# Performance work log

Measured on AMD Instinct MI355X. Metric: run time of the kernel, lower is better.

Reference implementation:

```python
import jax, jax.numpy as jnp
import numpy as np

DIM = 768
NUM_HEADS = 12
HEAD_DIM = DIM // NUM_HEADS
SCALE = HEAD_DIM ** -0.5
EPS = 1e-6


def setup_inputs() -> dict:
    key = jax.random.key(0)
    k_x, k_p, k_qkv, k_proj = jax.random.split(key, 4)
    B, N = 16, 577
    x = jax.random.normal(k_x, (B, N, DIM), dtype=jnp.float32)
    # binary keep/drop policy per token (as produced by an upstream gumbel gate)
    policy = jax.random.randint(k_p, (B, N, 1), 0, 2).astype(jnp.float32)
    Wqkv = jax.random.normal(k_qkv, (DIM, 3 * DIM), dtype=jnp.float32) * 0.02
    bqkv = jnp.zeros((3 * DIM,), dtype=jnp.float32)
    Wproj = jax.random.normal(k_proj, (DIM, DIM), dtype=jnp.float32) * 0.02
    bproj = jnp.zeros((DIM,), dtype=jnp.float32)
    return {"x": x, "policy": policy, "Wqkv": Wqkv, "bqkv": bqkv,
            "Wproj": Wproj, "bproj": bproj}


def reference(x, policy, Wqkv, bqkv, Wproj, bproj):
    B, N, C = x.shape
    # qkv projection -> [3, B, H, N, Dh]
    qkv = (x @ Wqkv + bqkv).reshape(B, N, 3, NUM_HEADS, HEAD_DIM)
    qkv = jnp.transpose(qkv, (2, 0, 3, 1, 4))
    q, k, v = qkv[0], qkv[1], qkv[2]
    # scaled attention logits [B, H, N, N]
    attn = jnp.einsum("bhnd,bhmd->bhnm", q, k) * SCALE
    # policy-masked softmax (training-mode formula: eye keeps self-attention alive)
    ap = policy.reshape(B, 1, 1, N)
    eye = jnp.eye(N, dtype=ap.dtype).reshape(1, 1, N, N)
    ap = ap + (1.0 - ap) * eye
    max_att = jnp.max(attn, axis=-1, keepdims=True)
    e = jnp.exp(attn - max_att) * ap
    attn = (e + EPS / N) / (jnp.sum(e, axis=-1, keepdims=True) + EPS)
    # attend and project
    out = jnp.einsum("bhnm,bhmd->bhnd", attn, v)
    out = jnp.transpose(out, (0, 2, 1, 3)).reshape(B, N, C)
    return out @ Wproj + bproj
```

## Files before the change

kernel.cpp:

```cpp
#include <hip/hip_runtime.h>
#include <hip/hip_bf16.h>

#define QKVC   2304
#define NHEAD  12
#define NTOK   577
#define NBATCH 16
#define NROWS  (NBATCH * NTOK)
#define NPAD   640
#define SCALE  0.125f
#define EPSV   1e-6f

typedef __bf16  bf16x8 __attribute__((ext_vector_type(8)));
typedef float   f32x4  __attribute__((ext_vector_type(4)));

__device__ __forceinline__ unsigned short f2bf(float f) {
    union { float f; unsigned u; } v; v.f = f;
    unsigned r = v.u + 0x7FFFu + ((v.u >> 16) & 1u);
    return (unsigned short)(r >> 16);
}
__device__ __forceinline__ unsigned short f2bf_trunc(float f) {
    return (unsigned short)(__float_as_uint(f) >> 16);
}
__device__ __forceinline__ f32x4 mfma16(bf16x8 a, bf16x8 b, f32x4 c) {
    return __builtin_amdgcn_mfma_f32_16x16x32_bf16(a, b, c, 0, 0, 0);
}

#define GLDS16(g, l) __builtin_amdgcn_global_load_lds( \
    (const __attribute__((address_space(1))) unsigned int*)(g), \
    (__attribute__((address_space(3))) unsigned int*)(l), 16, 0, 0)

__device__ void transpose_tile(const float* __restrict__ src, unsigned short* __restrict__ dst,
                               int K, int N, int bx, int by, int t) {
    __shared__ unsigned short lt[64 * 72];
    int n0 = bx * 64, k0 = by * 64;
    int kk = t >> 4, nn = (t & 15) * 4;
    for (int i = 0; i < 4; i++) {
        int kr = kk + i * 16;
        float4 v = *(const float4*)&src[(size_t)(k0 + kr) * N + n0 + nn];
        lt[(nn + 0) * 72 + kr] = f2bf(v.x);
        lt[(nn + 1) * 72 + kr] = f2bf(v.y);
        lt[(nn + 2) * 72 + kr] = f2bf(v.z);
        lt[(nn + 3) * 72 + kr] = f2bf(v.w);
    }
    __syncthreads();
    int n = t >> 2, seg = (t & 3) * 16;
    uint4 a = *(uint4*)&lt[n * 72 + seg];
    uint4 b = *(uint4*)&lt[n * 72 + seg + 8];
    *(uint4*)&dst[(size_t)(n0 + n) * K + k0 + seg]     = a;
    *(uint4*)&dst[(size_t)(n0 + n) * K + k0 + seg + 8] = b;
}

#define NCONV (NROWS * 768 / 4 / 256)
__global__ void k_prep(const float* __restrict__ x, unsigned short* __restrict__ xb,
                       const float* __restrict__ Wqkv, unsigned short* __restrict__ wqkvt,
                       const float* __restrict__ Wproj, unsigned short* __restrict__ wprojt) {
    int id = blockIdx.x, t = threadIdx.x;
    if (id < NCONV) {
        int idx = id * 256 + t;
        float4 v = ((const float4*)x)[idx];
        ushort4 o;
        o.x = f2bf(v.x); o.y = f2bf(v.y); o.z = f2bf(v.z); o.w = f2bf(v.w);
        ((ushort4*)xb)[idx] = o;
    } else if (id < NCONV + 432) {
        int i2 = id - NCONV;
        transpose_tile(Wqkv, wqkvt, 768, QKVC, i2 % 36, i2 / 36, t);
    } else {
        int i2 = id - NCONV - 432;
        transpose_tile(Wproj, wprojt, 768, 768, i2 % 12, i2 / 12, t);
    }
}

template <bool F32OUT>
__global__ __launch_bounds__(512, 2)
void k_gemm(const unsigned short* __restrict__ A, const unsigned short* __restrict__ B,
            const float* __restrict__ bias, void* __restrict__ outp, int Ncols,
            unsigned short* __restrict__ vt) {
    __shared__ unsigned short SL[49152];
    int t = threadIdx.x;
    int lane = t & 63, wave = t >> 6, quad = lane >> 4, l15 = lane & 15;
    int wm = wave >> 2, wn = wave & 3;
    int nT = Ncols >> 7;
    int nwg = gridDim.x;

    int q8 = nwg >> 3, r8 = nwg & 7;
    int xcd = blockIdx.x & 7, idx = blockIdx.x >> 3;
    int wg = (xcd < r8 ? xcd * (q8 + 1) : r8 * (q8 + 1) + (xcd - r8) * q8) + idx;
    int m0 = (wg / nT) * 256;
    int n0 = (wg % nT) * 128;

    int srow = lane >> 2;
    int sseg = (lane & 3) ^ ((lane >> 3) & 3);
    const unsigned short* gA0 = A + (size_t)(m0 +       wave * 16 + srow) * 768 + sseg * 8;
    const unsigned short* gA1 = A + (size_t)(m0 + 128 + wave * 16 + srow) * 768 + sseg * 8;
    const unsigned short* gB0 = B + (size_t)(n0 +       wave * 16 + srow) * 768 + sseg * 8;

    f32x4 acc[8][2] = {};

    auto STAGE = [&](int sx) {
        unsigned sa = (unsigned)(sx & 3) * 8192u + (unsigned)wave * 512u;
        unsigned sb = 32768u + (unsigned)(sx & 3) * 4096u + (unsigned)wave * 512u;
        int ko = sx * 32;
        GLDS16(gA0 + ko, &SL[sa]);
        GLDS16(gA1 + ko, &SL[sa + 4096]);
        GLDS16(gB0 + ko, &SL[sb]);
    };

    auto STEP = [&](int s, bool stage) {
        unsigned ab = (unsigned)(s & 3) * 8192u;
        unsigned bb = 32768u + (unsigned)(s & 3) * 4096u;
        unsigned ro = (unsigned)(quad ^ ((l15 >> 1) & 3)) * 8u;
        bf16x8 af[8], bfr[2];
        #pragma unroll
        for (int i = 0; i < 8; i++)
            af[i]  = *(const bf16x8*)&SL[ab + (unsigned)(wm * 128 + i * 16 + l15) * 32u + ro];
        #pragma unroll
        for (int i = 0; i < 2; i++)
            bfr[i] = *(const bf16x8*)&SL[bb + (unsigned)(wn * 32 + i * 16 + l15) * 32u + ro];
        if (stage) STAGE(s + 3);
        asm volatile("s_waitcnt lgkmcnt(0)" ::: "memory");
        __builtin_amdgcn_s_setprio(1);
        #pragma unroll
        for (int mi = 0; mi < 8; mi++)
            #pragma unroll
            for (int ni = 0; ni < 2; ni++)
                acc[mi][ni] = mfma16(af[mi], bfr[ni], acc[mi][ni]);
        __builtin_amdgcn_s_setprio(0);
    };

    STAGE(0); STAGE(1); STAGE(2);
    for (int s = 0; s < 21; s++) {
        asm volatile("s_waitcnt vmcnt(6)" ::: "memory");
        asm volatile("s_barrier" ::: "memory");
        STEP(s, true);
    }
    asm volatile("s_waitcnt vmcnt(6)" ::: "memory");
    asm volatile("s_barrier" ::: "memory");
    STEP(21, false);
    asm volatile("s_waitcnt vmcnt(3)" ::: "memory");
    asm volatile("s_barrier" ::: "memory");
    STEP(22, false);
    asm volatile("s_waitcnt vmcnt(0)" ::: "memory");
    asm volatile("s_barrier" ::: "memory");
    STEP(23, false);

    if constexpr (F32OUT) {
        for (int ni = 0; ni < 2; ni++) {
            int col = n0 + wn * 32 + ni * 16 + l15;
            float bv = bias[col];
            for (int mi = 0; mi < 8; mi++) {
                int rowm = m0 + wm * 128 + mi * 16 + quad * 4;
                for (int r = 0; r < 4; r++) {
                    int m = rowm + r;
                    if (m < NROWS)
                        ((float*)outp)[(size_t)m * Ncols + col] = acc[mi][ni][r] + bv;
                }
            }
        }
    } else {
        __syncthreads();
        for (int ni = 0; ni < 2; ni++) {
            int colL = wn * 32 + ni * 16 + l15;
            float bv = bias[n0 + colL];
            for (int mi = 0; mi < 8; mi++) {
                int rowL = wm * 128 + mi * 16 + quad * 4;
                for (int r = 0; r < 4; r++)
                    SL[(rowL + r) * 136 + colL] = f2bf(acc[mi][ni][r] + bv);
            }
        }
        __syncthreads();
        if (n0 < 1536) {
            for (int rr = 0; rr < 8; rr++) {
                int row = rr * 32 + (t >> 4);
                int m = m0 + row;
                if (m < NROWS) {
                    uint4 v = *(uint4*)&SL[row * 136 + (t & 15) * 8];
                    *(uint4*)&((unsigned short*)outp)[(size_t)m * Ncols + n0 + (t & 15) * 8] = v;
                }
            }
        } else {
            int h0 = (n0 - 1536) >> 6;
            for (int i = 0; i < 16; i++) {
                int c = wave * 16 + i;
                int h = h0 + (c >> 6), d = c & 63;
                for (int half = 0; half < 4; half++) {
                    int lr = half * 64 + lane;
                    int m = m0 + lr;
                    if (m < NROWS) {
                        unsigned bbx = (unsigned)m / 577u;
                        int tok = m - (int)bbx * 577;
                        vt[(((size_t)bbx * NHEAD + h) * 64 + d) * NPAD + tok] =
                            SL[lr * 136 + c];
                    }
                }
            }
        }
    }
}

__global__ __launch_bounds__(256, 4)
void k_attn(const unsigned short* __restrict__ qkv, const unsigned short* __restrict__ vt,
            const float* __restrict__ policy, unsigned short* __restrict__ ao) {
    __shared__ unsigned short Ks[64 * 72];
    __shared__ unsigned short Vs[64 * 72];
    __shared__ unsigned short Ps[4][32 * 72];
    __shared__ float pol[NPAD];
    int t = threadIdx.x;
    int lane = t & 63, wave = t >> 6, quad = lane >> 4, l15 = lane & 15;
    int b = blockIdx.z, h = blockIdx.y, qt = blockIdx.x;
    const unsigned short* qbase = qkv + (size_t)(b * NTOK) * QKVC + h * 64;
    const unsigned short* kbase = qkv + (size_t)(b * NTOK) * QKVC + 768 + h * 64;
    const unsigned short* vbase = vt + (size_t)(b * NHEAD + h) * 64 * NPAD;

    for (int i = t; i < NPAD; i += 256)
        pol[i] = (i < NTOK) ? policy[b * NTOK + i] : 0.f;

    bf16x8 qf[2][2];
    for (int mi = 0; mi < 2; mi++) {
        const unsigned short* qp =
            qbase + (size_t)(qt * 128 + mi * 64 + wave * 16 + l15) * QKVC + quad * 8;
        qf[mi][0] = *(const bf16x8*)qp;
        qf[mi][1] = *(const bf16x8*)(qp + 32);
    }
    bf16x8 onesf;
    for (int j = 0; j < 8; j++) onesf[j] = (__bf16)1.0f;
    f32x4 o[2][4] = {};
    f32x4 ls[2] = {};
    int rowtok0[2];
    for (int mi = 0; mi < 2; mi++)
        rowtok0[mi] = qt * 128 + mi * 64 + wave * 16 + quad * 4;
    __syncthreads();

    for (int kt = 0; kt < 10; kt++) {
        int key0 = kt * 64;
        for (int i = t; i < 512; i += 256) {
            int row = i >> 3, seg = (i & 7) * 8;
            *(uint4*)&Ks[row * 72 + seg] = *(const uint4*)&kbase[(size_t)(key0 + row) * QKVC + seg];
            *(uint4*)&Vs[row * 72 + seg] = *(const uint4*)&vbase[(size_t)row * NPAD + key0 + seg];
        }
        __syncthreads();

        for (int ci = 0; ci < 4; ci++) {
            bf16x8 kf0 = *(const bf16x8*)&Ks[(ci * 16 + l15) * 72 + quad * 8];
            bf16x8 kf1 = *(const bf16x8*)&Ks[(ci * 16 + l15) * 72 + 32 + quad * 8];
            int col = key0 + ci * 16 + l15;
            float pc = pol[col];
            for (int mi = 0; mi < 2; mi++) {
                f32x4 a = {};
                a = mfma16(qf[mi][0], kf0, a);
                a = mfma16(qf[mi][1], kf1, a);
                for (int r = 0; r < 4; r++) {
                    float ap = (col == rowtok0[mi] + r) ? 1.f : pc;
                    float e = __expf(a[r] * SCALE) * ap;
                    Ps[wave][(mi * 16 + quad * 4 + r) * 72 + ci * 16 + l15] = f2bf_trunc(e);
                }
            }
        }
        __asm__ volatile("s_waitcnt lgkmcnt(0)" ::: "memory");
        bf16x8 pf[2][2];
        for (int mi = 0; mi < 2; mi++) {
            pf[mi][0] = *(const bf16x8*)&Ps[wave][(mi * 16 + l15) * 72 + quad * 8];
            pf[mi][1] = *(const bf16x8*)&Ps[wave][(mi * 16 + l15) * 72 + 32 + quad * 8];
            ls[mi] = mfma16(pf[mi][0], onesf, ls[mi]);
            ls[mi] = mfma16(pf[mi][1], onesf, ls[mi]);
        }
        for (int di = 0; di < 4; di++) {
            bf16x8 vf0 = *(const bf16x8*)&Vs[(di * 16 + l15) * 72 + quad * 8];
            bf16x8 vf1 = *(const bf16x8*)&Vs[(di * 16 + l15) * 72 + 32 + quad * 8];
            for (int mi = 0; mi < 2; mi++) {
                o[mi][di] = mfma16(pf[mi][0], vf0, o[mi][di]);
                o[mi][di] = mfma16(pf[mi][1], vf1, o[mi][di]);
            }
        }
        __syncthreads();
    }

    for (int mi = 0; mi < 2; mi++) {
        for (int r = 0; r < 4; r++) {
            int tok = rowtok0[mi] + r;
            if (tok < NTOK) {
                float inv = __builtin_amdgcn_rcpf(ls[mi][r] + EPSV);
                for (int di = 0; di < 4; di++) {
                    float val = o[mi][di][r] * inv;
                    ao[((size_t)(b * NTOK + tok)) * 768 + h * 64 + di * 16 + l15] = f2bf(val);
                }
            }
        }
    }
}

extern "C" void kernel_launch(void* const* d_in, const int* in_sizes, int n_in,
                              void* d_out, int out_size, void* d_ws, size_t ws_size,
                              hipStream_t stream) {
    const float* x      = (const float*)d_in[0];
    const float* policy = (const float*)d_in[1];
    const float* Wqkv   = (const float*)d_in[2];
    const float* bqkv   = (const float*)d_in[3];
    const float* Wproj  = (const float*)d_in[4];
    const float* bproj  = (const float*)d_in[5];
    float* out = (float*)d_out;

    unsigned short* p = (unsigned short*)d_ws;
    unsigned short* xb     = p;
    unsigned short* ao     = p; p += (size_t)NROWS * 768;
    unsigned short* wqkvt  = p; p += (size_t)QKVC * 768;
    unsigned short* wprojt = p; p += (size_t)768 * 768;
    unsigned short* qkvb   = p; p += (size_t)NROWS * QKVC;
    unsigned short* vt     = p; p += (size_t)NBATCH * NHEAD * 64 * NPAD;

    int mT = (NROWS + 255) / 256;

    k_prep<<<NCONV + 432 + 144, 256, 0, stream>>>(x, xb, Wqkv, wqkvt, Wproj, wprojt);
    k_gemm<false><<<mT * (QKVC / 128), 512, 0, stream>>>(
        xb, wqkvt, bqkv, (void*)qkvb, QKVC, vt);
    k_attn<<<dim3(NPAD / 128, NHEAD, NBATCH), 256, 0, stream>>>(qkvb, vt, policy, ao);
    k_gemm<true><<<mT * (768 / 128), 512, 0, stream>>>(
        ao, wprojt, bproj, (void*)out, 768, nullptr);
}
```

Before: 206.7 us.

## Pre-tile GEMM operands into swizzled 16x32 chunks and use triple-buffered staging

The x conversion, weight transposes and the attention output now write GEMM operands in a pre-tiled, pre-swizzled layout of contiguous 16-row by 32-k chunks. Each wave's global-to-LDS load then reads one contiguous 1 KB block instead of strided row segments. The GEMM pipeline drops from four LDS stages to three, which cuts LDS use and may allow more occupancy, at the cost of less prefetch depth. The attention epilogue now does scattered scalar stores into the tiled layout.

```diff
diff --git a/kernel.cpp b/kernel.cpp
--- a/kernel.cpp
+++ b/kernel.cpp
@@ -9,6 +9,8 @@
 #define NPAD   640
 #define SCALE  0.125f
 #define EPSV   1e-6f
+#define KT     24
+#define CH     512
 
 typedef __bf16  bf16x8 __attribute__((ext_vector_type(8)));
 typedef float   f32x4  __attribute__((ext_vector_type(4)));
@@ -21,6 +23,9 @@
 __device__ __forceinline__ unsigned short f2bf_trunc(float f) {
     return (unsigned short)(__float_as_uint(f) >> 16);
 }
+__device__ __forceinline__ unsigned pack2bf(float a, float b) {
+    return (unsigned)f2bf(a) | ((unsigned)f2bf(b) << 16);
+}
 __device__ __forceinline__ f32x4 mfma16(bf16x8 a, bf16x8 b, f32x4 c) {
     return __builtin_amdgcn_mfma_f32_16x16x32_bf16(a, b, c, 0, 0, 0);
 }
@@ -29,8 +34,9 @@
     (const __attribute__((address_space(1))) unsigned int*)(g), \
     (__attribute__((address_space(3))) unsigned int*)(l), 16, 0, 0)
 
+
 __device__ void transpose_tile(const float* __restrict__ src, unsigned short* __restrict__ dst,
-                               int K, int N, int bx, int by, int t) {
+                               int N, int bx, int by, int t) {
     __shared__ unsigned short lt[64 * 72];
     int n0 = bx * 64, k0 = by * 64;
     int kk = t >> 4, nn = (t & 15) * 4;
@@ -43,30 +49,52 @@
         lt[(nn + 3) * 72 + kr] = f2bf(v.w);
     }
     __syncthreads();
-    int n = t >> 2, seg = (t & 3) * 16;
-    uint4 a = *(uint4*)&lt[n * 72 + seg];
-    uint4 b = *(uint4*)&lt[n * 72 + seg + 8];
-    *(uint4*)&dst[(size_t)(n0 + n) * K + k0 + seg]     = a;
-    *(uint4*)&dst[(size_t)(n0 + n) * K + k0 + seg + 8] = b;
-}
-
-#define NCONV (NROWS * 768 / 4 / 256)
-__global__ void k_prep(const float* __restrict__ x, unsigned short* __restrict__ xb,
+    int n = t >> 2;
+    int ks = (t & 3) * 16;
+    int gn = n0 + n;
+    int ntile = gn >> 4, r = gn & 15, s = (r >> 1) & 3;
+    for (int j = 0; j < 2; j++) {
+        int k = k0 + ks + j * 8;
+        int kt = k >> 5;
+        int q = ((k >> 3) & 3) ^ s;
+        uint4 v = *(uint4*)&lt[n * 72 + ks + j * 8];
+        *(uint4*)&dst[((size_t)ntile * KT + kt) * CH + r * 32 + q * 8] = v;
+    }
+}
+
+#define NCHUNK (577 * KT)
+#define CONVB  ((NCHUNK + 15) / 16)
+__global__ void k_prep(const float* __restrict__ x, unsigned short* __restrict__ xbt,
                        const float* __restrict__ Wqkv, unsigned short* __restrict__ wqkvt,
                        const float* __restrict__ Wproj, unsigned short* __restrict__ wprojt) {
     int id = blockIdx.x, t = threadIdx.x;
-    if (id < NCONV) {
-        int idx = id * 256 + t;
-        float4 v = ((const float4*)x)[idx];
-        ushort4 o;
-        o.x = f2bf(v.x); o.y = f2bf(v.y); o.z = f2bf(v.z); o.w = f2bf(v.w);
-        ((ushort4*)xb)[idx] = o;
-    } else if (id < NCONV + 432) {
-        int i2 = id - NCONV;
-        transpose_tile(Wqkv, wqkvt, 768, QKVC, i2 % 36, i2 / 36, t);
+    if (id < CONVB) {
+        int cid = id * 16 + (t >> 4);
+        if (cid < NCHUNK) {
+            int r = t & 15;
+            int mt = cid / KT, kt = cid - mt * KT;
+            const float* src = x + ((size_t)mt * 16 + r) * 768 + kt * 32;
+            int s = (r >> 1) & 3;
+            unsigned short* dst = xbt + (size_t)cid * CH + r * 32;
+            #pragma unroll
+            for (int q = 0; q < 4; q++) {
+                int g = q ^ s;
+                float4 v0 = *(const float4*)(src + g * 8);
+                float4 v1 = *(const float4*)(src + g * 8 + 4);
+                uint4 u;
+                u.x = pack2bf(v0.x, v0.y);
+                u.y = pack2bf(v0.z, v0.w);
+                u.z = pack2bf(v1.x, v1.y);
+                u.w = pack2bf(v1.z, v1.w);
+                *(uint4*)(dst + q * 8) = u;
+            }
+        }
+    } else if (id < CONVB + 432) {
+        int i2 = id - CONVB;
+        transpose_tile(Wqkv, wqkvt, QKVC, i2 % 36, i2 / 36, t);
     } else {
-        int i2 = id - NCONV - 432;
-        transpose_tile(Wproj, wprojt, 768, 768, i2 % 12, i2 / 12, t);
+        int i2 = id - CONVB - 432;
+        transpose_tile(Wproj, wprojt, 768, i2 % 12, i2 / 12, t);
     }
 }
 
@@ -75,7 +103,7 @@
 void k_gemm(const unsigned short* __restrict__ A, const unsigned short* __restrict__ B,
             const float* __restrict__ bias, void* __restrict__ outp, int Ncols,
             unsigned short* __restrict__ vt) {
-    __shared__ unsigned short SL[49152];
+    __shared__ unsigned short SL[36864];
     int t = threadIdx.x;
     int lane = t & 63, wave = t >> 6, quad = lane >> 4, l15 = lane & 15;
     int wm = wave >> 2, wn = wave & 3;
@@ -88,26 +116,23 @@
     int m0 = (wg / nT) * 256;
     int n0 = (wg % nT) * 128;
 
-    int srow = lane >> 2;
-    int sseg = (lane & 3) ^ ((lane >> 3) & 3);
-    const unsigned short* gA0 = A + (size_t)(m0 +       wave * 16 + srow) * 768 + sseg * 8;
-    const unsigned short* gA1 = A + (size_t)(m0 + 128 + wave * 16 + srow) * 768 + sseg * 8;
-    const unsigned short* gB0 = B + (size_t)(n0 +       wave * 16 + srow) * 768 + sseg * 8;
+    const unsigned short* gA0 = A + ((size_t)((m0 >> 4) + wave) * KT) * CH + lane * 8;
+    const unsigned short* gA1 = gA0 + (size_t)8 * KT * CH;
+    const unsigned short* gB0 = B + ((size_t)((n0 >> 4) + wave) * KT) * CH + lane * 8;
 
     f32x4 acc[8][2] = {};
 
-    auto STAGE = [&](int sx) {
-        unsigned sa = (unsigned)(sx & 3) * 8192u + (unsigned)wave * 512u;
-        unsigned sb = 32768u + (unsigned)(sx & 3) * 4096u + (unsigned)wave * 512u;
-        int ko = sx * 32;
-        GLDS16(gA0 + ko, &SL[sa]);
-        GLDS16(gA1 + ko, &SL[sa + 4096]);
-        GLDS16(gB0 + ko, &SL[sb]);
+    auto STAGE = [&](int sx, unsigned slot) {
+        unsigned sa = slot * 8192u + (unsigned)wave * 512u;
+        unsigned sb = 24576u + slot * 4096u + (unsigned)wave * 512u;
+        GLDS16(gA0 + sx * CH, &SL[sa]);
+        GLDS16(gA1 + sx * CH, &SL[sa + 4096]);
+        GLDS16(gB0 + sx * CH, &SL[sb]);
     };
 
-    auto STEP = [&](int s, bool stage) {
-        unsigned ab = (unsigned)(s & 3) * 8192u;
-        unsigned bb = 32768u + (unsigned)(s & 3) * 4096u;
+    auto STEP = [&](unsigned slot, int sx, unsigned sslot, bool stage) {
+        unsigned ab = slot * 8192u;
+        unsigned bb = 24576u + slot * 4096u;
         unsigned ro = (unsigned)(quad ^ ((l15 >> 1) & 3)) * 8u;
         bf16x8 af[8], bfr[2];
         #pragma unroll
@@ -116,7 +141,7 @@
         #pragma unroll
         for (int i = 0; i < 2; i++)
             bfr[i] = *(const bf16x8*)&SL[bb + (unsigned)(wn * 32 + i * 16 + l15) * 32u + ro];
-        if (stage) STAGE(s + 3);
+        if (stage) STAGE(sx, sslot);
         asm volatile("s_waitcnt lgkmcnt(0)" ::: "memory");
         __builtin_amdgcn_s_setprio(1);
         #pragma unroll
@@ -127,21 +152,15 @@
         __builtin_amdgcn_s_setprio(0);
     };
 
-    STAGE(0); STAGE(1); STAGE(2);
-    for (int s = 0; s < 21; s++) {
-        asm volatile("s_waitcnt vmcnt(6)" ::: "memory");
+    STAGE(0, 0); STAGE(1, 1);
+    for (int s = 0; s < 23; s++) {
+        asm volatile("s_waitcnt vmcnt(3)" ::: "memory");
         asm volatile("s_barrier" ::: "memory");
-        STEP(s, true);
-    }
-    asm volatile("s_waitcnt vmcnt(6)" ::: "memory");
-    asm volatile("s_barrier" ::: "memory");
-    STEP(21, false);
-    asm volatile("s_waitcnt vmcnt(3)" ::: "memory");
-    asm volatile("s_barrier" ::: "memory");
-    STEP(22, false);
+        STEP((unsigned)(s % 3), s + 2, (unsigned)((s + 2) % 3), s < 22);
+    }
     asm volatile("s_waitcnt vmcnt(0)" ::: "memory");
     asm volatile("s_barrier" ::: "memory");
-    STEP(23, false);
+    STEP(2u, 0, 0u, false);
 
     if constexpr (F32OUT) {
         for (int ni = 0; ni < 2; ni++) {
@@ -279,9 +298,15 @@
             int tok = rowtok0[mi] + r;
             if (tok < NTOK) {
                 float inv = __builtin_amdgcn_rcpf(ls[mi][r] + EPSV);
+                int m = b * NTOK + tok;
+                int mt = m >> 4, rr = m & 15, s = (rr >> 1) & 3;
+                unsigned short* dst = ao + ((size_t)mt * KT) * CH + rr * 32;
                 for (int di = 0; di < 4; di++) {
-                    float val = o[mi][di][r] * inv;
-                    ao[((size_t)(b * NTOK + tok)) * 768 + h * 64 + di * 16 + l15] = f2bf(val);
+                    int k = h * 64 + di * 16 + l15;
+                    int kt2 = k >> 5;
+                    int q = ((k >> 3) & 3) ^ s;
+                    dst[(size_t)kt2 * CH + q * 8 + (l15 & 7)] =
+                        f2bf(o[mi][di][r] * inv);
                 }
             }
         }
@@ -309,7 +334,7 @@
 
     int mT = (NROWS + 255) / 256;
 
-    k_prep<<<NCONV + 432 + 144, 256, 0, stream>>>(x, xb, Wqkv, wqkvt, Wproj, wprojt);
+    k_prep<<<CONVB + 432 + 144, 256, 0, stream>>>(x, xb, Wqkv, wqkvt, Wproj, wprojt);
     k_gemm<false><<<mT * (QKVC / 128), 512, 0, stream>>>(
         xb, wqkvt, bqkv, (void*)qkvb, QKVC, vt);
     k_attn<<<dim3(NPAD / 128, NHEAD, NBATCH), 256, 0, stream>>>(qkvb, vt, policy, ao);
```

After: 191.0 us. -7.6%, faster.
